# Kernel optimization log

Measured on AMD Instinct MI355X. Metric: run time of the kernel, lower is better.

Reference implementation:

```python
import jax, jax.numpy as jnp
import numpy as np

DIM = 32  # fixed internal node dim
N_GRAPHS = 64


def setup_inputs() -> dict:
    key = jax.random.key(0)
    ks = jax.random.split(key, 16)
    N, E, F_N, F_E, H = 12500, 200000, 16, 8, 32
    inp = {
        "x": jax.random.normal(ks[0], (N, F_N), dtype=jnp.float32),
        "edge_index": jax.random.randint(ks[1], (2, E), 0, N, dtype=jnp.int64),
        "edge_attr": jax.random.normal(ks[2], (E, F_E), dtype=jnp.float32),
        "batch": jnp.sort(jax.random.randint(ks[3], (N,), 0, N_GRAPHS, dtype=jnp.int64)),
        "lin0_w": jax.random.normal(ks[4], (DIM, F_N), dtype=jnp.float32) * 0.1,
        "lin0_b": jax.random.normal(ks[5], (DIM,), dtype=jnp.float32) * 0.1,
        "nn_w": jax.random.normal(ks[6], (DIM * H, F_E), dtype=jnp.float32) * 0.1,
        "nn_b": jax.random.normal(ks[7], (DIM * H,), dtype=jnp.float32) * 0.1,
        "root_w": jax.random.normal(ks[8], (DIM, H), dtype=jnp.float32) * 0.1,
        "conv_b": jax.random.normal(ks[9], (H,), dtype=jnp.float32) * 0.1,
        "lin1_w": jax.random.normal(ks[10], (16, H), dtype=jnp.float32) * 0.1,
        "lin1_b": jax.random.normal(ks[11], (16,), dtype=jnp.float32) * 0.1,
        "lin2_w": jax.random.normal(ks[12], (1, 16), dtype=jnp.float32) * 0.1,
        "lin2_b": jax.random.normal(ks[13], (1,), dtype=jnp.float32) * 0.1,
    }
    return inp


def reference(x, edge_index, edge_attr, batch, lin0_w, lin0_b, nn_w, nn_b,
              root_w, conv_b, lin1_w, lin1_b, lin2_w, lin2_b):
    N = x.shape[0]
    H = conv_b.shape[0]
    # lin0 + relu -> node features [N, DIM]
    out = jax.nn.relu(x @ lin0_w.T + lin0_b)
    # NNConv: per-edge weight matrices from edge MLP (single Linear)
    src, dst = edge_index[0], edge_index[1]
    w_e = (edge_attr @ nn_w.T + nn_b).reshape(-1, DIM, H)  # [E, DIM, H]
    msg = jnp.einsum('ed,edh->eh', out[src], w_e)          # gather + per-edge matmul
    agg = jax.ops.segment_sum(msg, dst, num_segments=N)     # scatter-add
    h = jax.nn.relu(agg + out @ root_w + conv_b)             # root weight + bias
    # global add pool over graphs
    u = jax.ops.segment_sum(h, batch, num_segments=N_GRAPHS)  # [G, H]
    o = jax.nn.relu(u @ lin1_w.T + lin1_b)
    o = o @ lin2_w.T + lin2_b
    return o.reshape(-1)
```

## Files before the change

### kernel.cpp

```cpp
#include <hip/hip_runtime.h>

#define DIMN 32
#define HD   32
#define FN   16
#define FE   8
#define NG   64
#define CAP  64
#define K3T  512
#define K3W  (K3T / 64)

__global__ __launch_bounds__(256) void k1_out(
    const float* __restrict__ x, const float* __restrict__ lin0_w,
    const float* __restrict__ lin0_b,
    float* __restrict__ outn, float* __restrict__ aggfb, float* __restrict__ u,
    int* __restrict__ deg, int* __restrict__ done, int N)
{
    const int gt = blockIdx.x * 256 + threadIdx.x;
    if (gt >= N * DIMN) return;
    const int n = gt >> 5, d = gt & 31;

    float s = lin0_b[d];
    const float* xr = x + (size_t)n * FN;
    const float* wr = lin0_w + d * FN;
    #pragma unroll
    for (int j = 0; j < FN; ++j) s = fmaf(xr[j], wr[j], s);
    outn[gt] = fmaxf(s, 0.f);

    aggfb[gt] = 0.f;
    if (d == 0) deg[n] = 0;
    if (gt < NG * HD) u[gt] = 0.f;
    if (gt == 0) *done = 0;
}

__global__ __launch_bounds__(256) void kb_bucket(
    const int* __restrict__ ei, const float* __restrict__ ea,
    const float* __restrict__ outn, const float* __restrict__ nn_w,
    const float* __restrict__ nn_b,
    int* __restrict__ deg, int2* __restrict__ es, float* __restrict__ aggfb, int E)
{
    const int e = blockIdx.x * 256 + threadIdx.x;
    if (e >= E) return;
    const int src = ei[e];
    const int dst = ei[E + e];
    const int pos = atomicAdd(&deg[dst], 1);
    if (pos < CAP) {
        es[(size_t)dst * CAP + pos] = make_int2(e, src);
    } else {
        float ef[FE];
        #pragma unroll
        for (int f = 0; f < FE; ++f) ef[f] = ea[(size_t)e * FE + f];
        for (int h = 0; h < HD; ++h) {
            float m = 0.f;
            for (int d = 0; d < DIMN; ++d) {
                float wdh = nn_b[d * HD + h];
                #pragma unroll
                for (int f = 0; f < FE; ++f)
                    wdh = fmaf(ef[f], nn_w[(d * HD + h) * FE + f], wdh);
                m = fmaf(outn[(size_t)src * DIMN + d], wdh, m);
            }
            atomicAdd(aggfb + (size_t)dst * HD + h, m);
        }
    }
}

#define EDGE_FMA(o, a) \
    S  = (S + (o));                      \
    T0 = fmaf((o), (a).x, T0);           \
    T1 = fmaf((o), (a).y, T1);           \
    T2 = fmaf((o), (a).z, T2);           \
    T3 = fmaf((o), (a).w, T3);

#define CONTRIB(DD, A) { \
    const int d_ = d0 + (DD); \
    const float4 ta_ = *(const float4*)&s_T[w * 256 + d_ * 8]; \
    const float4 tb_ = *(const float4*)&s_T[w * 256 + d_ * 8 + 4]; \
    const float2 so_ = s_SO[w * 32 + d_]; \
    const int b_ = d_ * 256 + h; \
    A = fmaf(ta_.x, s_nnw2[b_      ], A); \
    A = fmaf(ta_.y, s_nnw2[b_ +  32], A); \
    A = fmaf(ta_.z, s_nnw2[b_ +  64], A); \
    A = fmaf(ta_.w, s_nnw2[b_ +  96], A); \
    A = fmaf(tb_.x, s_nnw2[b_ + 128], A); \
    A = fmaf(tb_.y, s_nnw2[b_ + 160], A); \
    A = fmaf(tb_.z, s_nnw2[b_ + 192], A); \
    A = fmaf(tb_.w, s_nnw2[b_ + 224], A); \
    A = fmaf(so_.x, s_nnb[d_ * 32 + h], A); \
    A = fmaf(so_.y, s_rw [d_ * 32 + h], A); }

__global__ __launch_bounds__(K3T, 8) void k3_gather(
    const float* __restrict__ ea, const float* __restrict__ outn,
    const int2* __restrict__ es, const float* __restrict__ nn_w,
    const float* __restrict__ nn_b, const float* __restrict__ root_w,
    const float* __restrict__ conv_b, const int* __restrict__ deg,
    const float* __restrict__ aggfb, const int* __restrict__ batch,
    const float* __restrict__ lin1_w, const float* __restrict__ lin1_b,
    const float* __restrict__ lin2_w, const float* __restrict__ lin2_b,
    float* __restrict__ u, int* __restrict__ done, float* __restrict__ outp,
    int N, int nblocks)
{
    __shared__ float  s_nnw2[DIMN * FE * HD];
    __shared__ float  s_nnb[DIMN * HD];
    __shared__ float  s_rw[DIMN * HD];
    __shared__ float  s_cb[HD];
    __shared__ float  s_T[K3W * 256];
    __shared__ float2 s_SO[K3W * 32];
    __shared__ float  s_V[K3W * 32];
    __shared__ int    s_G[K3W];
    __shared__ int    s_last;

    const int tid = threadIdx.x;
    for (int i = tid; i < DIMN * FE * HD; i += K3T) {
        const int d = i >> 8, rem = i & 255, hh = rem >> 3, f = rem & 7;
        s_nnw2[(d * 8 + f) * 32 + hh] = nn_w[i];
    }
    for (int i = tid; i < DIMN * HD; i += K3T) { s_nnb[i] = nn_b[i]; s_rw[i] = root_w[i]; }
    if (tid < HD) s_cb[tid] = conv_b[tid];
    __syncthreads();

    const int l = tid & 63;
    const int h = l & 31;
    const int p = l >> 5;
    const int w = tid >> 6;
    const int n = blockIdx.x * K3W + w;

    int gval = -1;
    if (n < N) {
        const int nu = __builtin_amdgcn_readfirstlane(n);
        const int dn = min(deg[nu], CAP);
        const int2* ep = es + (size_t)nu * CAP;
        const int f0 = 4 * p;

        float T0 = 0.f, T1 = 0.f, T2 = 0.f, T3 = 0.f, S = 0.f;

        for (int j0 = 0; j0 < dn; j0 += 8) {
            const int jm = dn - 1;
            const int2 E0 = ep[j0];
            const int2 E1 = ep[min(j0 + 1, jm)];
            const int2 E2 = ep[min(j0 + 2, jm)];
            const int2 E3 = ep[min(j0 + 3, jm)];
            const int2 E4 = ep[min(j0 + 4, jm)];
            const int2 E5 = ep[min(j0 + 5, jm)];
            const int2 E6 = ep[min(j0 + 6, jm)];
            const int2 E7 = ep[min(j0 + 7, jm)];

            const float4 a0 = *(const float4*)(ea + (size_t)E0.x * FE + f0);
            const float4 a1 = *(const float4*)(ea + (size_t)E1.x * FE + f0);
            const float4 a2 = *(const float4*)(ea + (size_t)E2.x * FE + f0);
            const float4 a3 = *(const float4*)(ea + (size_t)E3.x * FE + f0);
            const float4 a4 = *(const float4*)(ea + (size_t)E4.x * FE + f0);
            const float4 a5 = *(const float4*)(ea + (size_t)E5.x * FE + f0);
            const float4 a6 = *(const float4*)(ea + (size_t)E6.x * FE + f0);
            const float4 a7 = *(const float4*)(ea + (size_t)E7.x * FE + f0);
            float o0 = outn[(size_t)E0.y * DIMN + h];
            float o1 = outn[(size_t)E1.y * DIMN + h];
            float o2 = outn[(size_t)E2.y * DIMN + h];
            float o3 = outn[(size_t)E3.y * DIMN + h];
            float o4 = outn[(size_t)E4.y * DIMN + h];
            float o5 = outn[(size_t)E5.y * DIMN + h];
            float o6 = outn[(size_t)E6.y * DIMN + h];
            float o7 = outn[(size_t)E7.y * DIMN + h];

            o1 = (j0 + 1 <= jm) ? o1 : 0.f;
            o2 = (j0 + 2 <= jm) ? o2 : 0.f;
            o3 = (j0 + 3 <= jm) ? o3 : 0.f;
            o4 = (j0 + 4 <= jm) ? o4 : 0.f;
            o5 = (j0 + 5 <= jm) ? o5 : 0.f;
            o6 = (j0 + 6 <= jm) ? o6 : 0.f;
            o7 = (j0 + 7 <= jm) ? o7 : 0.f;

            EDGE_FMA(o0, a0) EDGE_FMA(o1, a1) EDGE_FMA(o2, a2) EDGE_FMA(o3, a3)
            EDGE_FMA(o4, a4) EDGE_FMA(o5, a5) EDGE_FMA(o6, a6) EDGE_FMA(o7, a7)
        }

        *(float4*)&s_T[w * 256 + h * 8 + f0] = make_float4(T0, T1, T2, T3);
        if (p == 0) s_SO[w * 32 + h] = make_float2(S, outn[(size_t)nu * DIMN + h]);

        const float base = aggfb[(size_t)nu * HD + h] + s_cb[h];

        float acc0 = 0.f, acc1 = 0.f, acc2 = 0.f, acc3 = 0.f;
        const int d0 = p << 4;
        #pragma unroll
        for (int dd = 0; dd < 16; dd += 4) {
            CONTRIB(dd + 0, acc0)
            CONTRIB(dd + 1, acc1)
            CONTRIB(dd + 2, acc2)
            CONTRIB(dd + 3, acc3)
        }
        float acc = (acc0 + acc1) + (acc2 + acc3);
        acc += __shfl_xor(acc, 32);

        const float v = fmaxf(acc + base, 0.f);
        if (p == 0) s_V[w * 32 + h] = v;
        gval = batch[nu];
    }
    if (l == 0) s_G[w] = gval;
    __syncthreads();

    if (tid < 32) {
        float accp = 0.f;
        int   gc   = -1;
        #pragma unroll
        for (int ww = 0; ww < K3W; ++ww) {
            const int gg = s_G[ww];
            if (gg >= 0) {
                const float vv = s_V[ww * 32 + tid];
                if (gg != gc) {
                    if (gc >= 0) atomicAdd(u + (size_t)gc * HD + tid, accp);
                    gc = gg;
                    accp = vv;
                } else {
                    accp += vv;
                }
            }
        }
        if (gc >= 0) atomicAdd(u + (size_t)gc * HD + tid, accp);
    }

    if (tid < 64) asm volatile("s_waitcnt vmcnt(0)" ::: "memory");
    __syncthreads();
    if (tid == 0) s_last = (atomicAdd(done, 1) == nblocks - 1) ? 1 : 0;
    __syncthreads();
    if (s_last && tid < NG) {
        const int g = tid;
        float ur[HD];
        #pragma unroll
        for (int hh = 0; hh < HD; ++hh)
            ur[hh] = atomicAdd(&u[(size_t)g * HD + hh], 0.f);
        float acc2 = lin2_b[0];
        #pragma unroll
        for (int i = 0; i < 16; ++i) {
            float o = lin1_b[i];
            #pragma unroll
            for (int hh = 0; hh < HD; ++hh)
                o = fmaf(ur[hh], lin1_w[i * HD + hh], o);
            o = fmaxf(o, 0.f);
            acc2 = fmaf(o, lin2_w[i], acc2);
        }
        outp[g] = acc2;
    }
}

extern "C" void kernel_launch(void* const* d_in, const int* in_sizes, int n_in,
                              void* d_out, int out_size, void* d_ws, size_t ws_size,
                              hipStream_t stream)
{
    const float* x      = (const float*)d_in[0];
    const int*   ei     = (const int*)  d_in[1];
    const float* ea     = (const float*)d_in[2];
    const int*   batch  = (const int*)  d_in[3];
    const float* lin0_w = (const float*)d_in[4];
    const float* lin0_b = (const float*)d_in[5];
    const float* nn_w   = (const float*)d_in[6];
    const float* nn_b   = (const float*)d_in[7];
    const float* root_w = (const float*)d_in[8];
    const float* conv_b = (const float*)d_in[9];
    const float* lin1_w = (const float*)d_in[10];
    const float* lin1_b = (const float*)d_in[11];
    const float* lin2_w = (const float*)d_in[12];
    const float* lin2_b = (const float*)d_in[13];

    const int N = in_sizes[0] / FN;
    const int E = in_sizes[2] / FE;

    float* ws    = (float*)d_ws;
    float* outn  = ws;
    float* aggfb = outn  + (size_t)N * DIMN;
    float* u     = aggfb + (size_t)N * DIMN;
    int*   deg   = (int*)(u + (size_t)NG * HD);
    int2*  es    = (int2*)(deg + N);
    int*   done  = (int*)(es + (size_t)N * CAP);

    const int nb1 = (N * DIMN + 255) / 256;
    k1_out<<<nb1, 256, 0, stream>>>(x, lin0_w, lin0_b, outn, aggfb, u, deg, done, N);

    const int nbb = (E + 255) / 256;
    kb_bucket<<<nbb, 256, 0, stream>>>(ei, ea, outn, nn_w, nn_b, deg, es, aggfb, E);

    const int nb3 = (N + K3W - 1) / K3W;
    k3_gather<<<nb3, K3T, 0, stream>>>(ea, outn, es, nn_w, nn_b, root_w, conv_b,
                                       deg, aggfb, batch,
                                       lin1_w, lin1_b, lin2_w, lin2_b,
                                       u, done, (float*)d_out, N, nb3);
}
```

Baseline: 147.8 us.

## Fuse three kernels into one persistent kernel with grid-wide barriers

Replaces the three launches (node linear, edge bucketing, gather/aggregate) with a single persistent kernel of 512 blocks that separates phases with atomic-counter grid barriers, plus a memset of the counter. Each block processes 16 nodes per unit in two passes of 8 warps and keeps a running per-graph partial sum across them. Edge bucket entries are packed into 64-bit words written with atomicExch so the writes are visible across blocks. The goal is to remove launch gaps and per-kernel setup. In exchange it adds spin-barrier cost, atomic stores in place of plain stores, lower parallelism in the early phases, and a deadlock risk if the 512 blocks cannot all be resident at once.

```diff
diff --git a/kernel.cpp b/kernel.cpp
--- a/kernel.cpp
+++ b/kernel.cpp
@@ -6,69 +6,26 @@
 #define FE   8
 #define NG   64
 #define CAP  64
-#define K3T  512
-#define K3W  (K3T / 64)
-
-__global__ __launch_bounds__(256) void k1_out(
-    const float* __restrict__ x, const float* __restrict__ lin0_w,
-    const float* __restrict__ lin0_b,
-    float* __restrict__ outn, float* __restrict__ aggfb, float* __restrict__ u,
-    int* __restrict__ deg, int* __restrict__ done, int N)
-{
-    const int gt = blockIdx.x * 256 + threadIdx.x;
-    if (gt >= N * DIMN) return;
-    const int n = gt >> 5, d = gt & 31;
-
-    float s = lin0_b[d];
-    const float* xr = x + (size_t)n * FN;
-    const float* wr = lin0_w + d * FN;
-    #pragma unroll
-    for (int j = 0; j < FN; ++j) s = fmaf(xr[j], wr[j], s);
-    outn[gt] = fmaxf(s, 0.f);
-
-    aggfb[gt] = 0.f;
-    if (d == 0) deg[n] = 0;
-    if (gt < NG * HD) u[gt] = 0.f;
-    if (gt == 0) *done = 0;
+#define BLK  512
+#define GRID 512
+#define KW   8
+#define NPU  16
+
+__device__ __forceinline__ void phase_barrier(int* cnt, int target) {
+    asm volatile("s_waitcnt vmcnt(0)" ::: "memory");
+    __syncthreads();
+    if (threadIdx.x == 0) {
+        atomicAdd(cnt, 1);
+        while (atomicAdd(cnt, 0) < target)
+            __builtin_amdgcn_s_sleep(16);
+    }
+    __syncthreads();
 }
 
-__global__ __launch_bounds__(256) void kb_bucket(
-    const int* __restrict__ ei, const float* __restrict__ ea,
-    const float* __restrict__ outn, const float* __restrict__ nn_w,
-    const float* __restrict__ nn_b,
-    int* __restrict__ deg, int2* __restrict__ es, float* __restrict__ aggfb, int E)
-{
-    const int e = blockIdx.x * 256 + threadIdx.x;
-    if (e >= E) return;
-    const int src = ei[e];
-    const int dst = ei[E + e];
-    const int pos = atomicAdd(&deg[dst], 1);
-    if (pos < CAP) {
-        es[(size_t)dst * CAP + pos] = make_int2(e, src);
-    } else {
-        float ef[FE];
-        #pragma unroll
-        for (int f = 0; f < FE; ++f) ef[f] = ea[(size_t)e * FE + f];
-        for (int h = 0; h < HD; ++h) {
-            float m = 0.f;
-            for (int d = 0; d < DIMN; ++d) {
-                float wdh = nn_b[d * HD + h];
-                #pragma unroll
-                for (int f = 0; f < FE; ++f)
-                    wdh = fmaf(ef[f], nn_w[(d * HD + h) * FE + f], wdh);
-                m = fmaf(outn[(size_t)src * DIMN + d], wdh, m);
-            }
-            atomicAdd(aggfb + (size_t)dst * HD + h, m);
-        }
-    }
-}
-
 #define EDGE_FMA(o, a) \
-    S  = (S + (o));                      \
-    T0 = fmaf((o), (a).x, T0);           \
-    T1 = fmaf((o), (a).y, T1);           \
-    T2 = fmaf((o), (a).z, T2);           \
-    T3 = fmaf((o), (a).w, T3);
+    S += (o); \
+    T0 = fmaf((o), (a).x, T0);  T1 = fmaf((o), (a).y, T1); \
+    T2 = fmaf((o), (a).z, T2);  T3 = fmaf((o), (a).w, T3);
 
 #define CONTRIB(DD, A) { \
     const int d_ = d0 + (DD); \
@@ -87,140 +44,193 @@
     A = fmaf(so_.x, s_nnb[d_ * 32 + h], A); \
     A = fmaf(so_.y, s_rw [d_ * 32 + h], A); }
 
-__global__ __launch_bounds__(K3T, 8) void k3_gather(
-    const float* __restrict__ ea, const float* __restrict__ outn,
-    const int2* __restrict__ es, const float* __restrict__ nn_w,
-    const float* __restrict__ nn_b, const float* __restrict__ root_w,
-    const float* __restrict__ conv_b, const int* __restrict__ deg,
-    const float* __restrict__ aggfb, const int* __restrict__ batch,
+__global__ __launch_bounds__(BLK, 4) void mega_fused(
+    const float* __restrict__ x, const int* __restrict__ ei,
+    const float* __restrict__ ea, const int* __restrict__ batch,
+    const float* __restrict__ lin0_w, const float* __restrict__ lin0_b,
+    const float* __restrict__ nn_w, const float* __restrict__ nn_b,
+    const float* __restrict__ root_w, const float* __restrict__ conv_b,
     const float* __restrict__ lin1_w, const float* __restrict__ lin1_b,
     const float* __restrict__ lin2_w, const float* __restrict__ lin2_b,
-    float* __restrict__ u, int* __restrict__ done, float* __restrict__ outp,
-    int N, int nblocks)
+    float* __restrict__ outn, float* __restrict__ aggfb, float* __restrict__ u,
+    int* __restrict__ deg, unsigned long long* __restrict__ esll,
+    int* __restrict__ cnt, float* __restrict__ outp, int N, int E)
 {
     __shared__ float  s_nnw2[DIMN * FE * HD];
     __shared__ float  s_nnb[DIMN * HD];
     __shared__ float  s_rw[DIMN * HD];
     __shared__ float  s_cb[HD];
-    __shared__ float  s_T[K3W * 256];
-    __shared__ float2 s_SO[K3W * 32];
-    __shared__ float  s_V[K3W * 32];
-    __shared__ int    s_G[K3W];
-    __shared__ int    s_last;
+    __shared__ float  s_T[KW * 256];
+    __shared__ float2 s_SO[KW * 32];
+    __shared__ float  s_V[KW * 32];
+    __shared__ int    s_G[KW];
 
     const int tid = threadIdx.x;
-    for (int i = tid; i < DIMN * FE * HD; i += K3T) {
+
+    for (int i = tid; i < DIMN * FE * HD; i += BLK) {
         const int d = i >> 8, rem = i & 255, hh = rem >> 3, f = rem & 7;
         s_nnw2[(d * 8 + f) * 32 + hh] = nn_w[i];
     }
-    for (int i = tid; i < DIMN * HD; i += K3T) { s_nnb[i] = nn_b[i]; s_rw[i] = root_w[i]; }
+    for (int i = tid; i < DIMN * HD; i += BLK) { s_nnb[i] = nn_b[i]; s_rw[i] = root_w[i]; }
     if (tid < HD) s_cb[tid] = conv_b[tid];
-    __syncthreads();
+
+    for (int gt = blockIdx.x * BLK + tid; gt < N * DIMN; gt += GRID * BLK) {
+        const int n = gt >> 5, d = gt & 31;
+        float s = lin0_b[d];
+        const float* xr = x + (size_t)n * FN;
+        const float* wr = lin0_w + d * FN;
+        #pragma unroll
+        for (int j = 0; j < FN; ++j) s = fmaf(xr[j], wr[j], s);
+        atomicExch(&outn[gt], fmaxf(s, 0.f));
+        atomicExch(&aggfb[gt], 0.f);
+        if (d == 0) atomicExch(&deg[n], 0);
+    }
+    if (blockIdx.x == 0)
+        for (int i = tid; i < NG * HD; i += BLK) atomicExch(&u[i], 0.f);
+
+    phase_barrier(cnt, GRID);
+
+    for (int e = blockIdx.x * BLK + tid; e < E; e += GRID * BLK) {
+        const int src = ei[e];
+        const int dst = ei[E + e];
+        const int pos = atomicAdd(&deg[dst], 1);
+        if (pos < CAP) {
+            atomicExch(&esll[(size_t)dst * CAP + pos],
+                       ((unsigned long long)(unsigned)src << 32) | (unsigned)e);
+        } else {
+            float ef[FE];
+            #pragma unroll
+            for (int f = 0; f < FE; ++f) ef[f] = ea[(size_t)e * FE + f];
+            for (int hh = 0; hh < HD; ++hh) {
+                float m = 0.f;
+                for (int d = 0; d < DIMN; ++d) {
+                    float wdh = nn_b[d * HD + hh];
+                    #pragma unroll
+                    for (int f = 0; f < FE; ++f)
+                        wdh = fmaf(ef[f], nn_w[(d * HD + hh) * FE + f], wdh);
+                    m = fmaf(outn[(size_t)src * DIMN + d], wdh, m);
+                }
+                atomicAdd(aggfb + (size_t)dst * HD + hh, m);
+            }
+        }
+    }
+    phase_barrier(cnt, 2 * GRID);
 
     const int l = tid & 63;
     const int h = l & 31;
     const int p = l >> 5;
     const int w = tid >> 6;
-    const int n = blockIdx.x * K3W + w;
-
-    int gval = -1;
-    if (n < N) {
-        const int nu = __builtin_amdgcn_readfirstlane(n);
-        const int dn = min(deg[nu], CAP);
-        const int2* ep = es + (size_t)nu * CAP;
-        const int f0 = 4 * p;
-
-        float T0 = 0.f, T1 = 0.f, T2 = 0.f, T3 = 0.f, S = 0.f;
-
-        for (int j0 = 0; j0 < dn; j0 += 8) {
-            const int jm = dn - 1;
-            const int2 E0 = ep[j0];
-            const int2 E1 = ep[min(j0 + 1, jm)];
-            const int2 E2 = ep[min(j0 + 2, jm)];
-            const int2 E3 = ep[min(j0 + 3, jm)];
-            const int2 E4 = ep[min(j0 + 4, jm)];
-            const int2 E5 = ep[min(j0 + 5, jm)];
-            const int2 E6 = ep[min(j0 + 6, jm)];
-            const int2 E7 = ep[min(j0 + 7, jm)];
-
-            const float4 a0 = *(const float4*)(ea + (size_t)E0.x * FE + f0);
-            const float4 a1 = *(const float4*)(ea + (size_t)E1.x * FE + f0);
-            const float4 a2 = *(const float4*)(ea + (size_t)E2.x * FE + f0);
-            const float4 a3 = *(const float4*)(ea + (size_t)E3.x * FE + f0);
-            const float4 a4 = *(const float4*)(ea + (size_t)E4.x * FE + f0);
-            const float4 a5 = *(const float4*)(ea + (size_t)E5.x * FE + f0);
-            const float4 a6 = *(const float4*)(ea + (size_t)E6.x * FE + f0);
-            const float4 a7 = *(const float4*)(ea + (size_t)E7.x * FE + f0);
-            float o0 = outn[(size_t)E0.y * DIMN + h];
-            float o1 = outn[(size_t)E1.y * DIMN + h];
-            float o2 = outn[(size_t)E2.y * DIMN + h];
-            float o3 = outn[(size_t)E3.y * DIMN + h];
-            float o4 = outn[(size_t)E4.y * DIMN + h];
-            float o5 = outn[(size_t)E5.y * DIMN + h];
-            float o6 = outn[(size_t)E6.y * DIMN + h];
-            float o7 = outn[(size_t)E7.y * DIMN + h];
-
-            o1 = (j0 + 1 <= jm) ? o1 : 0.f;
-            o2 = (j0 + 2 <= jm) ? o2 : 0.f;
-            o3 = (j0 + 3 <= jm) ? o3 : 0.f;
-            o4 = (j0 + 4 <= jm) ? o4 : 0.f;
-            o5 = (j0 + 5 <= jm) ? o5 : 0.f;
-            o6 = (j0 + 6 <= jm) ? o6 : 0.f;
-            o7 = (j0 + 7 <= jm) ? o7 : 0.f;
-
-            EDGE_FMA(o0, a0) EDGE_FMA(o1, a1) EDGE_FMA(o2, a2) EDGE_FMA(o3, a3)
-            EDGE_FMA(o4, a4) EDGE_FMA(o5, a5) EDGE_FMA(o6, a6) EDGE_FMA(o7, a7)
+    const int nunits = (N + NPU - 1) / NPU;
+
+    for (int unit = blockIdx.x; unit < nunits; unit += GRID) {
+        float accp  = 0.f;
+        int   g_cur = -1;
+        for (int it = 0; it < 2; ++it) {
+            const int n = unit * NPU + it * KW + w;
+            int gval = -1;
+            if (n < N) {
+                const int nu = __builtin_amdgcn_readfirstlane(n);
+                const int dn = min(deg[nu], CAP);
+                const unsigned long long* ep = esll + (size_t)nu * CAP;
+                const int f0 = 4 * p;
+
+                float T0 = 0.f, T1 = 0.f, T2 = 0.f, T3 = 0.f, S = 0.f;
+
+                for (int j0 = 0; j0 < dn; j0 += 8) {
+                    const int jm = dn - 1;
+                    const unsigned long long q0 = ep[j0];
+                    const unsigned long long q1 = ep[min(j0 + 1, jm)];
+                    const unsigned long long q2 = ep[min(j0 + 2, jm)];
+                    const unsigned long long q3 = ep[min(j0 + 3, jm)];
+                    const unsigned long long q4 = ep[min(j0 + 4, jm)];
+                    const unsigned long long q5 = ep[min(j0 + 5, jm)];
+                    const unsigned long long q6 = ep[min(j0 + 6, jm)];
+                    const unsigned long long q7 = ep[min(j0 + 7, jm)];
+                    const int e0 = (int)(unsigned)q0, s0 = (int)(q0 >> 32);
+                    const int e1 = (int)(unsigned)q1, s1 = (int)(q1 >> 32);
+                    const int e2 = (int)(unsigned)q2, s2 = (int)(q2 >> 32);
+                    const int e3 = (int)(unsigned)q3, s3 = (int)(q3 >> 32);
+                    const int e4 = (int)(unsigned)q4, s4 = (int)(q4 >> 32);
+                    const int e5 = (int)(unsigned)q5, s5 = (int)(q5 >> 32);
+                    const int e6 = (int)(unsigned)q6, s6 = (int)(q6 >> 32);
+                    const int e7 = (int)(unsigned)q7, s7 = (int)(q7 >> 32);
+
+                    const float4 a0 = *(const float4*)(ea + (size_t)e0 * FE + f0);
+                    const float4 a1 = *(const float4*)(ea + (size_t)e1 * FE + f0);
+                    const float4 a2 = *(const float4*)(ea + (size_t)e2 * FE + f0);
+                    const float4 a3 = *(const float4*)(ea + (size_t)e3 * FE + f0);
+                    const float4 a4 = *(const float4*)(ea + (size_t)e4 * FE + f0);
+                    const float4 a5 = *(const float4*)(ea + (size_t)e5 * FE + f0);
+                    const float4 a6 = *(const float4*)(ea + (size_t)e6 * FE + f0);
+                    const float4 a7 = *(const float4*)(ea + (size_t)e7 * FE + f0);
+                    float o0 = outn[(size_t)s0 * DIMN + h];
+                    float o1 = outn[(size_t)s1 * DIMN + h];
+                    float o2 = outn[(size_t)s2 * DIMN + h];
+                    float o3 = outn[(size_t)s3 * DIMN + h];
+                    float o4 = outn[(size_t)s4 * DIMN + h];
+                    float o5 = outn[(size_t)s5 * DIMN + h];
+                    float o6 = outn[(size_t)s6 * DIMN + h];
+                    float o7 = outn[(size_t)s7 * DIMN + h];
+
+                    o1 = (j0 + 1 <= jm) ? o1 : 0.f;
+                    o2 = (j0 + 2 <= jm) ? o2 : 0.f;
+                    o3 = (j0 + 3 <= jm) ? o3 : 0.f;
+                    o4 = (j0 + 4 <= jm) ? o4 : 0.f;
+                    o5 = (j0 + 5 <= jm) ? o5 : 0.f;
+                    o6 = (j0 + 6 <= jm) ? o6 : 0.f;
+                    o7 = (j0 + 7 <= jm) ? o7 : 0.f;
+
+                    EDGE_FMA(o0, a0) EDGE_FMA(o1, a1) EDGE_FMA(o2, a2) EDGE_FMA(o3, a3)
+                    EDGE_FMA(o4, a4) EDGE_FMA(o5, a5) EDGE_FMA(o6, a6) EDGE_FMA(o7, a7)
+                }
+
+                *(float4*)&s_T[w * 256 + h * 8 + f0] = make_float4(T0, T1, T2, T3);
+                if (p == 0) s_SO[w * 32 + h] = make_float2(S, outn[(size_t)nu * DIMN + h]);
+
+                const float base = aggfb[(size_t)nu * HD + h] + s_cb[h];
+
+                float acc0 = 0.f, acc1 = 0.f, acc2 = 0.f, acc3 = 0.f;
+                const int d0 = p << 4;
+                #pragma unroll
+                for (int dd = 0; dd < 16; dd += 4) {
+                    CONTRIB(dd + 0, acc0)
+                    CONTRIB(dd + 1, acc1)
+                    CONTRIB(dd + 2, acc2)
+                    CONTRIB(dd + 3, acc3)
+                }
+                float acc = (acc0 + acc1) + (acc2 + acc3);
+                acc += __shfl_xor(acc, 32);
+
+                const float v = fmaxf(acc + base, 0.f);
+                if (p == 0) s_V[w * 32 + h] = v;
+                gval = batch[nu];
+            }
+            if (l == 0) s_G[w] = gval;
+            __syncthreads();
+
+            if (tid < 32) {
+                #pragma unroll
+                for (int ww = 0; ww < KW; ++ww) {
+                    const int gg = s_G[ww];
+                    if (gg >= 0) {
+                        const float vv = s_V[ww * 32 + tid];
+                        if (gg != g_cur) {
+                            if (g_cur >= 0) atomicAdd(u + (size_t)g_cur * HD + tid, accp);
+                            g_cur = gg;
+                            accp = vv;
+                        } else {
+                            accp += vv;
+                        }
+                    }
+                }
+            }
+            __syncthreads();
         }
-
-        *(float4*)&s_T[w * 256 + h * 8 + f0] = make_float4(T0, T1, T2, T3);
-        if (p == 0) s_SO[w * 32 + h] = make_float2(S, outn[(size_t)nu * DIMN + h]);
-
-        const float base = aggfb[(size_t)nu * HD + h] + s_cb[h];
-
-        float acc0 = 0.f, acc1 = 0.f, acc2 = 0.f, acc3 = 0.f;
-        const int d0 = p << 4;
-        #pragma unroll
-        for (int dd = 0; dd < 16; dd += 4) {
-            CONTRIB(dd + 0, acc0)
-            CONTRIB(dd + 1, acc1)
-            CONTRIB(dd + 2, acc2)
-            CONTRIB(dd + 3, acc3)
-        }
-        float acc = (acc0 + acc1) + (acc2 + acc3);
-        acc += __shfl_xor(acc, 32);
-
-        const float v = fmaxf(acc + base, 0.f);
-        if (p == 0) s_V[w * 32 + h] = v;
-        gval = batch[nu];
-    }
-    if (l == 0) s_G[w] = gval;
-    __syncthreads();
-
-    if (tid < 32) {
-        float accp = 0.f;
-        int   gc   = -1;
-        #pragma unroll
-        for (int ww = 0; ww < K3W; ++ww) {
-            const int gg = s_G[ww];
-            if (gg >= 0) {
-                const float vv = s_V[ww * 32 + tid];
-                if (gg != gc) {
-                    if (gc >= 0) atomicAdd(u + (size_t)gc * HD + tid, accp);
-                    gc = gg;
-                    accp = vv;
-                } else {
-                    accp += vv;
-                }
-            }
-        }
-        if (gc >= 0) atomicAdd(u + (size_t)gc * HD + tid, accp);
-    }
-
-    if (tid < 64) asm volatile("s_waitcnt vmcnt(0)" ::: "memory");
-    __syncthreads();
-    if (tid == 0) s_last = (atomicAdd(done, 1) == nblocks - 1) ? 1 : 0;
-    __syncthreads();
-    if (s_last && tid < NG) {
+        if (tid < 32 && g_cur >= 0) atomicAdd(u + (size_t)g_cur * HD + tid, accp);
+    }
+    phase_barrier(cnt, 3 * GRID);
+
+    if (blockIdx.x == 0 && tid < NG) {
         const int g = tid;
         float ur[HD];
         #pragma unroll
@@ -262,23 +272,17 @@
     const int N = in_sizes[0] / FN;
     const int E = in_sizes[2] / FE;
 
-    float* ws    = (float*)d_ws;
-    float* outn  = ws;
+    int*   cnt   = (int*)d_ws;
+    float* outn  = (float*)d_ws + 16;
     float* aggfb = outn  + (size_t)N * DIMN;
     float* u     = aggfb + (size_t)N * DIMN;
     int*   deg   = (int*)(u + (size_t)NG * HD);
-    int2*  es    = (int2*)(deg + N);
-    int*   done  = (int*)(es + (size_t)N * CAP);
-
-    const int nb1 = (N * DIMN + 255) / 256;
-    k1_out<<<nb1, 256, 0, stream>>>(x, lin0_w, lin0_b, outn, aggfb, u, deg, done, N);
-
-    const int nbb = (E + 255) / 256;
-    kb_bucket<<<nbb, 256, 0, stream>>>(ei, ea, outn, nn_w, nn_b, deg, es, aggfb, E);
-
-    const int nb3 = (N + K3W - 1) / K3W;
-    k3_gather<<<nb3, K3T, 0, stream>>>(ea, outn, es, nn_w, nn_b, root_w, conv_b,
-                                       deg, aggfb, batch,
-                                       lin1_w, lin1_b, lin2_w, lin2_b,
-                                       u, done, (float*)d_out, N, nb3);
+    unsigned long long* esll = (unsigned long long*)(deg + N);
+
+    hipMemsetAsync(cnt, 0, 64, stream);
+
+    mega_fused<<<GRID, BLK, 0, stream>>>(
+        x, ei, ea, batch, lin0_w, lin0_b, nn_w, nn_b, root_w, conv_b,
+        lin1_w, lin1_b, lin2_w, lin2_b,
+        outn, aggfb, u, deg, esll, cnt, (float*)d_out, N, E);
 }
```

New measurement: 198.3 us. +34.2%, slower.
